# Performance work log

Hardware: AMD Instinct MI355X
Metric: run time of the kernel (lower is better)

The kernel has to match this reference:

```python
import jax, jax.numpy as jnp
import numpy as np

H = 32        # num_attention_heads
KVH = 8       # num_key_value_heads
D = 64        # head_dim
HID = 2048    # hidden_size
G = H // KVH  # num_key_value_groups


def setup_inputs() -> dict:
    key = jax.random.key(0)
    k1, k2, k3, k4, k5 = jax.random.split(key, 5)
    B, S = 1, 2048
    s = 1.0 / np.sqrt(HID)
    return {
        "hidden_states": jax.random.normal(k1, (B, S, HID), dtype=jnp.float32),
        "attention_mask": jnp.ones((B, S), dtype=jnp.int32),
        "Wq": jax.random.normal(k2, (H * D, HID), dtype=jnp.float32) * s,
        "Wk": jax.random.normal(k3, (KVH * D, HID), dtype=jnp.float32) * s,
        "Wv": jax.random.normal(k4, (KVH * D, HID), dtype=jnp.float32) * s,
        "Wo": jax.random.normal(k5, (HID, HID), dtype=jnp.float32) * s,
    }


def reference(hidden_states, attention_mask, Wq, Wk, Wv, Wo):
    B, S, _ = hidden_states.shape
    dtype = hidden_states.dtype

    q = (hidden_states @ Wq.T).reshape(B, S, H, D).transpose(0, 2, 1, 3)     # [B,H,S,D]
    k = (hidden_states @ Wk.T).reshape(B, S, KVH, D).transpose(0, 2, 1, 3)   # [B,KVH,S,D]
    v = (hidden_states @ Wv.T).reshape(B, S, KVH, D).transpose(0, 2, 1, 3)

    # repeat_interleave over head dim: each KV head serves G query heads
    k = jnp.repeat(k, G, axis=1)  # [B,H,S,D]
    v = jnp.repeat(v, G, axis=1)

    scores = jnp.einsum('bhqd,bhkd->bhqk', q, k) / np.sqrt(D)  # [B,H,S,S]

    causal = jnp.tril(jnp.ones((S, S), dtype=dtype))                # [S,S]
    am = attention_mask.astype(dtype)[:, None, None, :]              # [B,1,1,S]
    mask = am * causal[None, None, :, :]                             # [B,1,S,S]
    mask = (1.0 - mask) * jnp.finfo(dtype).min
    scores = scores + mask                                           # broadcast over heads

    weights = jax.nn.softmax(scores, axis=-1)
    attn = jnp.einsum('bhqk,bhkd->bhqd', weights, v)                 # [B,H,S,D]
    attn = attn.transpose(0, 2, 1, 3).reshape(B, S, HID)
    return attn @ Wo.T
```

## Files before the change

### kernel.cpp

```cpp
#include <hip/hip_runtime.h>
#include <hip/hip_bf16.h>
#include <math.h>

typedef __attribute__((ext_vector_type(4))) float f32x4;
typedef __attribute__((ext_vector_type(16))) float f32x16;
typedef __attribute__((ext_vector_type(8))) short bf16x8;
typedef __attribute__((ext_vector_type(4))) short s16x4;
typedef __attribute__((ext_vector_type(4))) unsigned int u32x4;
typedef __attribute__((ext_vector_type(2))) unsigned int u32x2;
typedef short s16;
typedef unsigned int u32;
typedef unsigned short u16;

#define S_LEN 2048
#define HIDN  2048
#define QKVW  3072
#define NH    32
#define NKVH  8
#define HD    64

__device__ __forceinline__ s16 f2bf(float f) {
  unsigned int u = __float_as_uint(f);
  unsigned int lsb = (u >> 16) & 1u;
  u += 0x7fffu + lsb;
  return (s16)(u >> 16);
}

__device__ __forceinline__ u32 cvtpk(float lo, float hi) {
  u32 r;
  asm("v_cvt_pk_bf16_f32 %0, %1, %2" : "=v"(r) : "v"(lo), "v"(hi));
  return r;
}

__device__ __forceinline__ void gload16(const void* g, void* l) {
  __builtin_amdgcn_global_load_lds(
      (const __attribute__((address_space(1))) void*)g,
      (__attribute__((address_space(3))) void*)l, 16, 0, 0);
}

__device__ __forceinline__ void pls(u32& a, u32& b) {
  asm volatile("v_permlane32_swap_b32 %0, %1" : "+v"(a), "+v"(b));
}

__device__ __forceinline__ int swz7(int row) { return (row ^ (row >> 3)) & 7; }

__global__ __launch_bounds__(256) void cvt_all(const float* __restrict__ h,
                                               const float* __restrict__ wq,
                                               const float* __restrict__ wk,
                                               const float* __restrict__ wv,
                                               const float* __restrict__ wo,
                                               s16x4* __restrict__ dst) {
  int i = blockIdx.x * 256 + threadIdx.x;
  const float* src; int off;
  if (i < 1048576)      { src = h;  off = i; }
  else if (i < 2097152) { src = wq; off = i - 1048576; }
  else if (i < 2359296) { src = wk; off = i - 2097152; }
  else if (i < 2621440) { src = wv; off = i - 2359296; }
  else                  { src = wo; off = i - 2621440; }
  if (i < 3670016) {
    float4 f = reinterpret_cast<const float4*>(src)[i < 1048576 ? i : off];
    s16x4 o;
    o.x = f2bf(f.x); o.y = f2bf(f.y); o.z = f2bf(f.z); o.w = f2bf(f.w);
    dst[i] = o;
  }
}

__device__ __forceinline__ void storeC(s16* C, size_t idx, float v)   { C[idx] = f2bf(v); }
__device__ __forceinline__ void storeC(float* C, size_t idx, float v) { C[idx] = v; }

template <typename OUT_T>
__global__ __launch_bounds__(512) void gemm_bt(const s16* __restrict__ A,
                                               const s16* __restrict__ B,
                                               OUT_T* __restrict__ C,
                                               int M, int N, int K) {
  __shared__ alignas(16) s16 As[2][8192];
  __shared__ alignas(16) s16 Bs[2][8192];

  const int t    = threadIdx.x;
  const int lane = t & 63;
  const int w    = t >> 6;
  const int wr   = (w >> 2) * 64;
  const int wc   = (w & 3) * 32;
  const int lr   = lane & 15;
  const int lg   = lane >> 4;
  const int bm   = blockIdx.y * 128;
  const int bn   = blockIdx.x * 128;

  const int srow0 = (w * 2) * 8 + (lane >> 3);
  const int srow1 = (w * 2 + 1) * 8 + (lane >> 3);
  const int sl0   = ((lane & 7) ^ swz7(srow0)) * 8;
  const int sl1   = ((lane & 7) ^ swz7(srow1)) * 8;

  f32x4 acc[4][2];
#pragma unroll
  for (int m = 0; m < 4; ++m)
#pragma unroll
    for (int n = 0; n < 2; ++n)
      acc[m][n] = (f32x4){0.f, 0.f, 0.f, 0.f};

  const int nK = K >> 6;
  int buf = 0;

  {
    gload16(&A[(size_t)(bm + srow0) * K + sl0], (char*)As[0] + (w * 2) * 1024);
    gload16(&A[(size_t)(bm + srow1) * K + sl1], (char*)As[0] + (w * 2 + 1) * 1024);
    gload16(&B[(size_t)(bn + srow0) * K + sl0], (char*)Bs[0] + (w * 2) * 1024);
    gload16(&B[(size_t)(bn + srow1) * K + sl1], (char*)Bs[0] + (w * 2 + 1) * 1024);
  }
  __syncthreads();

  for (int ki = 0; ki < nK; ++ki) {
    if (ki + 1 < nK) {
      const int kt = (ki + 1) << 6;
      gload16(&A[(size_t)(bm + srow0) * K + kt + sl0], (char*)As[buf ^ 1] + (w * 2) * 1024);
      gload16(&A[(size_t)(bm + srow1) * K + kt + sl1], (char*)As[buf ^ 1] + (w * 2 + 1) * 1024);
      gload16(&B[(size_t)(bn + srow0) * K + kt + sl0], (char*)Bs[buf ^ 1] + (w * 2) * 1024);
      gload16(&B[(size_t)(bn + srow1) * K + kt + sl1], (char*)Bs[buf ^ 1] + (w * 2 + 1) * 1024);
    }

    bf16x8 af[4][2], bfr[2][2];
#pragma unroll
    for (int kk = 0; kk < 2; ++kk) {
#pragma unroll
      for (int m = 0; m < 4; ++m) {
        int row = wr + m * 16 + lr;
        af[m][kk] = *(bf16x8*)((char*)As[buf] + row * 128 + (((kk * 4 + lg) ^ swz7(row)) << 4));
      }
#pragma unroll
      for (int n = 0; n < 2; ++n) {
        int row = wc + n * 16 + lr;
        bfr[n][kk] = *(bf16x8*)((char*)Bs[buf] + row * 128 + (((kk * 4 + lg) ^ swz7(row)) << 4));
      }
    }

    __builtin_amdgcn_s_setprio(1);
#pragma unroll
    for (int m = 0; m < 4; ++m)
#pragma unroll
      for (int n = 0; n < 2; ++n)
#pragma unroll
        for (int kk = 0; kk < 2; ++kk)
          acc[m][n] = __builtin_amdgcn_mfma_f32_16x16x32_bf16(af[m][kk], bfr[n][kk], acc[m][n], 0, 0, 0);
    __builtin_amdgcn_s_setprio(0);

    __syncthreads();
    buf ^= 1;
  }

#pragma unroll
  for (int m = 0; m < 4; ++m)
#pragma unroll
    for (int n = 0; n < 2; ++n) {
      int row = bm + wr + m * 16 + lg * 4;
      int col = bn + wc + n * 16 + lr;
#pragma unroll
      for (int j = 0; j < 4; ++j)
        storeC(C, (size_t)(row + j) * N + col, acc[m][n][j]);
    }
}

__global__ __launch_bounds__(256) void attn_kernel(
    const s16* __restrict__ QKV,
    const int* __restrict__ am,
    s16* __restrict__ Ob) {
  __shared__ alignas(16) char KsB[2][8192];
  __shared__ alignas(16) char VsB[2][8192];

  const int t    = threadIdx.x;
  const int lane = t & 63;
  const int w    = t >> 6;
  const int col  = lane & 31;
  const int hi   = lane >> 5;

  const int hk = blockIdx.x;
  const int qi = blockIdx.y;
  const int qt = (qi < 32) ? (63 - qi) : (qi - 32);
  const int h  = hk * 4 + w;
  const int nt = ((qt * 32 + 31) >> 6) + 1;
  const int kbase = 2048 + hk * 64;
  const int vbase = 2560 + hk * 64;

  const float CF = 0.18033688f;

  const int krow   = lane >> 3;
  const int kslotb = lane & 7;
  const int vkv    = 2 * (t >> 3);
  const int vd8    = (t & 7) * 8;

  const int qrow = qt * 32 + col;
  bf16x8 qf[4];
#pragma unroll
  for (int ds = 0; ds < 4; ++ds)
    qf[ds] = *(const bf16x8*)&QKV[(size_t)qrow * QKVW + h * 64 + ds * 16 + hi * 8];

  {
#pragma unroll
    for (int pp = 0; pp < 2; ++pp) {
      int c   = w * 2 + pp;
      int row = c * 8 + krow;
      int slot = kslotb ^ swz7(row);
      gload16(&QKV[(size_t)row * QKVW + kbase + slot * 8], KsB[0] + c * 1024);
    }
    bf16x8 va = *(const bf16x8*)&QKV[(size_t)vkv * QKVW + vbase + vd8];
    bf16x8 vb = *(const bf16x8*)&QKV[(size_t)(vkv + 1) * QKVW + vbase + vd8];
#pragma unroll
    for (int i = 0; i < 8; ++i) {
      int d = vd8 + i;
      u32 pk = (u32)(u16)va[i] | ((u32)(u16)vb[i] << 16);
      *(u32*)&VsB[0][(d * 128 + vkv * 2) ^ (swz7(d) << 4)] = pk;
    }
  }
  int acur = am[lane];

  float m_i = -1e30f, l_part = 0.f;
  f32x16 Oacc[2];
#pragma unroll
  for (int b = 0; b < 2; ++b)
#pragma unroll
    for (int i = 0; i < 16; ++i) Oacc[b][i] = 0.f;
  __syncthreads();

  for (int it = 0; it < nt; ++it) {
    const int cur = it & 1;
    const int kv0 = it * 64;
    const bool pre = (it + 1 < nt);

    bf16x8 va, vb;
    int anext = 0;
    if (pre) {
      const int nk0 = kv0 + 64;
#pragma unroll
      for (int pp = 0; pp < 2; ++pp) {
        int c   = w * 2 + pp;
        int row = c * 8 + krow;
        int slot = kslotb ^ swz7(row);
        gload16(&QKV[(size_t)(nk0 + row) * QKVW + kbase + slot * 8], KsB[cur ^ 1] + c * 1024);
      }
      va = *(const bf16x8*)&QKV[(size_t)(nk0 + vkv) * QKVW + vbase + vd8];
      vb = *(const bf16x8*)&QKV[(size_t)(nk0 + vkv + 1) * QKVW + vbase + vd8];
      anext = am[nk0 + lane];
    }

    f32x16 s0, s1;
#pragma unroll
    for (int i = 0; i < 16; ++i) { s0[i] = 0.f; s1[i] = 0.f; }
    __builtin_amdgcn_s_setprio(1);
#pragma unroll
    for (int ds = 0; ds < 4; ++ds) {
      int off = ds * 32 + hi * 16;
      bf16x8 k0 = *(bf16x8*)&KsB[cur][(col * 128 + off) ^ (swz7(col) << 4)];
      bf16x8 k1 = *(bf16x8*)&KsB[cur][((32 + col) * 128 + off) ^ (swz7(32 + col) << 4)];
      s0 = __builtin_amdgcn_mfma_f32_32x32x16_bf16(k0, qf[ds], s0, 0, 0, 0);
      s1 = __builtin_amdgcn_mfma_f32_32x32x16_bf16(k1, qf[ds], s1, 0, 0, 0);
    }
    __builtin_amdgcn_s_setprio(0);

    float pvv[32];
    unsigned long long m64 = __ballot(acur != 0);
    bool interior = (kv0 + 64 <= qt * 32) && (m64 == ~0ull);
    if (interior) {
#pragma unroll
      for (int r = 0; r < 16; ++r) { pvv[r] = s0[r] * CF; pvv[16 + r] = s1[r] * CF; }
    } else {
#pragma unroll
      for (int b = 0; b < 2; ++b)
#pragma unroll
        for (int r = 0; r < 16; ++r) {
          int kvl = b * 32 + (r & 3) + 8 * (r >> 2) + 4 * hi;
          float sv = b ? s1[r] : s0[r];
          bool ok = (kv0 + kvl <= qrow) && ((m64 >> kvl) & 1ull);
          pvv[b * 16 + r] = ok ? sv * CF : -INFINITY;
        }
    }

    float a0 = pvv[0], a1 = pvv[1], a2 = pvv[2], a3 = pvv[3];
#pragma unroll
    for (int i = 4; i < 32; i += 4) {
      a0 = fmaxf(a0, pvv[i]);     a1 = fmaxf(a1, pvv[i + 1]);
      a2 = fmaxf(a2, pvv[i + 2]); a3 = fmaxf(a3, pvv[i + 3]);
    }
    float lmax = fmaxf(fmaxf(a0, a1), fmaxf(a2, a3));
    lmax = fmaxf(lmax, __shfl_xor(lmax, 32));

    if (!__all(lmax - m_i <= 8.f)) {
      float nm = fmaxf(m_i, lmax);
      float al = __builtin_amdgcn_exp2f(m_i - nm);
      m_i = nm;
      l_part *= al;
#pragma unroll
      for (int b = 0; b < 2; ++b)
#pragma unroll
        for (int i = 0; i < 16; ++i) Oacc[b][i] *= al;
    }

    float t0 = 0.f, t1 = 0.f, t2 = 0.f, t3 = 0.f;
#pragma unroll
    for (int i = 0; i < 32; i += 4) {
      pvv[i]     = __builtin_amdgcn_exp2f(pvv[i] - m_i);     t0 += pvv[i];
      pvv[i + 1] = __builtin_amdgcn_exp2f(pvv[i + 1] - m_i); t1 += pvv[i + 1];
      pvv[i + 2] = __builtin_amdgcn_exp2f(pvv[i + 2] - m_i); t2 += pvv[i + 2];
      pvv[i + 3] = __builtin_amdgcn_exp2f(pvv[i + 3] - m_i); t3 += pvv[i + 3];
    }
    l_part += (t0 + t1) + (t2 + t3);

    bf16x8 pf[4];
#pragma unroll
    for (int b = 0; b < 2; ++b)
#pragma unroll
      for (int g = 0; g < 2; ++g) {
        int base = b * 16 + g * 8;
        u32 A1 = cvtpk(pvv[base + 0], pvv[base + 1]);
        u32 A2 = cvtpk(pvv[base + 2], pvv[base + 3]);
        u32 B1 = cvtpk(pvv[base + 4], pvv[base + 5]);
        u32 B2 = cvtpk(pvv[base + 6], pvv[base + 7]);
        pls(A1, B1);
        pls(A2, B2);
        u32x4 pw; pw[0] = A1; pw[1] = A2; pw[2] = B1; pw[3] = B2;
        pf[b * 2 + g] = *reinterpret_cast<bf16x8*>(&pw);
      }

    __builtin_amdgcn_s_setprio(1);
#pragma unroll
    for (int ks = 0; ks < 4; ++ks) {
      int off = ks * 32 + hi * 16;
#pragma unroll
      for (int db = 0; db < 2; ++db) {
        int d = db * 32 + col;
        bf16x8 vf = *(bf16x8*)&VsB[cur][(d * 128 + off) ^ (swz7(d) << 4)];
        Oacc[db] = __builtin_amdgcn_mfma_f32_32x32x16_bf16(vf, pf[ks], Oacc[db], 0, 0, 0);
      }
    }
    __builtin_amdgcn_s_setprio(0);

    if (pre) {
#pragma unroll
      for (int i = 0; i < 8; ++i) {
        int d = vd8 + i;
        u32 pk = (u32)(u16)va[i] | ((u32)(u16)vb[i] << 16);
        *(u32*)&VsB[cur ^ 1][(d * 128 + vkv * 2) ^ (swz7(d) << 4)] = pk;
      }
      acur = anext;
    }
    __syncthreads();
  }

  float l_i = l_part + __shfl_xor(l_part, 32);
  float linv = 1.0f / l_i;
#pragma unroll
  for (int db = 0; db < 2; ++db)
#pragma unroll
    for (int qd = 0; qd < 4; ++qd) {
      u32x2 o;
      o[0] = cvtpk(Oacc[db][qd * 4 + 0] * linv, Oacc[db][qd * 4 + 1] * linv);
      o[1] = cvtpk(Oacc[db][qd * 4 + 2] * linv, Oacc[db][qd * 4 + 3] * linv);
      int d0 = db * 32 + qd * 8 + hi * 4;
      *(u32x2*)&Ob[(size_t)qrow * HIDN + h * 64 + d0] = o;
    }
}

extern "C" void kernel_launch(void* const* d_in, const int* in_sizes, int n_in,
                              void* d_out, int out_size, void* d_ws, size_t ws_size,
                              hipStream_t stream) {
  const float* hidden = (const float*)d_in[0];
  const int*   am     = (const int*)d_in[1];
  const float* Wq     = (const float*)d_in[2];
  const float* Wk     = (const float*)d_in[3];
  const float* Wv     = (const float*)d_in[4];
  const float* Wo     = (const float*)d_in[5];
  float* out = (float*)d_out;

  s16* hb    = (s16*)d_ws;
  s16* wqkvb = hb    + 4194304;
  s16* wob   = wqkvb + 6291456;
  s16* QKVb  = wob   + 4194304;
  s16* Ab    = QKVb  + 6291456;

  cvt_all<<<14336, 256, 0, stream>>>(hidden, Wq, Wk, Wv, Wo, (s16x4*)d_ws);

  gemm_bt<s16><<<dim3(24, 16), 512, 0, stream>>>(hb, wqkvb, QKVb, 2048, 3072, 2048);

  attn_kernel<<<dim3(8, 64), 256, 0, stream>>>(QKVb, am, Ab);

  gemm_bt<float><<<dim3(16, 16), 512, 0, stream>>>(Ab, wob, out, 2048, 2048, 2048);
}
```

Measured before the change: 140.7 us.

## Split KV tiles across two wave groups per attention block and merge

The attention kernel now launches 512 threads per block. Two groups of four waves take alternating 64-row KV tiles, each with its own double-buffered K/V shared-memory region. At the end, group 0 writes its partial output, running max and sum to shared memory, and group 1 merges them with a log-sum-exp rescale before writing bf16 output. This halves the serial KV-loop length per block, which mainly helps the long causal rows, at the cost of double the LDS footprint, a final merge step and possibly lower block occupancy. A small cleanup also simplifies the source index in the fp32-to-bf16 conversion.

```diff
diff --git a/kernel.cpp b/kernel.cpp
--- a/kernel.cpp
+++ b/kernel.cpp
@@ -58,7 +58,7 @@
   else if (i < 2621440) { src = wv; off = i - 2359296; }
   else                  { src = wo; off = i - 2621440; }
   if (i < 3670016) {
-    float4 f = reinterpret_cast<const float4*>(src)[i < 1048576 ? i : off];
+    float4 f = reinterpret_cast<const float4*>(src)[off];
     s16x4 o;
     o.x = f2bf(f.x); o.y = f2bf(f.y); o.z = f2bf(f.z); o.w = f2bf(f.w);
     dst[i] = o;
@@ -159,16 +159,18 @@
     }
 }
 
-__global__ __launch_bounds__(256) void attn_kernel(
+__global__ __launch_bounds__(512) void attn_kernel(
     const s16* __restrict__ QKV,
     const int* __restrict__ am,
     s16* __restrict__ Ob) {
-  __shared__ alignas(16) char KsB[2][8192];
-  __shared__ alignas(16) char VsB[2][8192];
+  __shared__ alignas(16) char smem[65536];
+  __shared__ float2 mlb[4][64];
 
   const int t    = threadIdx.x;
+  const int g    = t >> 8;
+  const int tg   = t & 255;
   const int lane = t & 63;
-  const int w    = t >> 6;
+  const int w    = tg >> 6;
   const int col  = lane & 31;
   const int hi   = lane >> 5;
 
@@ -177,6 +179,7 @@
   const int qt = (qi < 32) ? (63 - qi) : (qi - 32);
   const int h  = hk * 4 + w;
   const int nt = ((qt * 32 + 31) >> 6) + 1;
+  const int R  = (nt + 1) >> 1;
   const int kbase = 2048 + hk * 64;
   const int vbase = 2560 + hk * 64;
 
@@ -184,8 +187,8 @@
 
   const int krow   = lane >> 3;
   const int kslotb = lane & 7;
-  const int vkv    = 2 * (t >> 3);
-  const int vd8    = (t & 7) * 8;
+  const int vkv    = 2 * (tg >> 3);
+  const int vd8    = (tg & 7) * 8;
 
   const int qrow = qt * 32 + col;
   bf16x8 qf[4];
@@ -193,24 +196,26 @@
   for (int ds = 0; ds < 4; ++ds)
     qf[ds] = *(const bf16x8*)&QKV[(size_t)qrow * QKVW + h * 64 + ds * 16 + hi * 8];
 
-  {
+  if (g < nt) {
+    char* Kn = smem + (g * 2 + 0) * 16384;
+    char* Vn = Kn + 8192;
 #pragma unroll
     for (int pp = 0; pp < 2; ++pp) {
       int c   = w * 2 + pp;
       int row = c * 8 + krow;
       int slot = kslotb ^ swz7(row);
-      gload16(&QKV[(size_t)row * QKVW + kbase + slot * 8], KsB[0] + c * 1024);
-    }
-    bf16x8 va = *(const bf16x8*)&QKV[(size_t)vkv * QKVW + vbase + vd8];
-    bf16x8 vb = *(const bf16x8*)&QKV[(size_t)(vkv + 1) * QKVW + vbase + vd8];
+      gload16(&QKV[(size_t)(g * 64 + row) * QKVW + kbase + slot * 8], Kn + c * 1024);
+    }
+    bf16x8 va = *(const bf16x8*)&QKV[(size_t)(g * 64 + vkv) * QKVW + vbase + vd8];
+    bf16x8 vb = *(const bf16x8*)&QKV[(size_t)(g * 64 + vkv + 1) * QKVW + vbase + vd8];
 #pragma unroll
     for (int i = 0; i < 8; ++i) {
       int d = vd8 + i;
       u32 pk = (u32)(u16)va[i] | ((u32)(u16)vb[i] << 16);
-      *(u32*)&VsB[0][(d * 128 + vkv * 2) ^ (swz7(d) << 4)] = pk;
-    }
-  }
-  int acur = am[lane];
+      *(u32*)&Vn[(d * 128 + vkv * 2) ^ (swz7(d) << 4)] = pk;
+    }
+  }
+  int acur = am[g * 64 + lane];
 
   float m_i = -1e30f, l_part = 0.f;
   f32x16 Oacc[2];
@@ -220,142 +225,173 @@
     for (int i = 0; i < 16; ++i) Oacc[b][i] = 0.f;
   __syncthreads();
 
-  for (int it = 0; it < nt; ++it) {
-    const int cur = it & 1;
-    const int kv0 = it * 64;
-    const bool pre = (it + 1 < nt);
+  for (int it = 0; it < R; ++it) {
+    const int buf  = it & 1;
+    const int tile = 2 * it + g;
+    const bool valid = (tile < nt);
+    const int kv0  = tile * 64;
+    const bool pre = (tile + 2 < nt);
+
+    char* Kc = smem + (g * 2 + buf) * 16384;
+    char* Vc = Kc + 8192;
+    char* Kn = smem + (g * 2 + (buf ^ 1)) * 16384;
+    char* Vn = Kn + 8192;
 
     bf16x8 va, vb;
     int anext = 0;
     if (pre) {
-      const int nk0 = kv0 + 64;
+      const int nk0 = kv0 + 128;
 #pragma unroll
       for (int pp = 0; pp < 2; ++pp) {
         int c   = w * 2 + pp;
         int row = c * 8 + krow;
         int slot = kslotb ^ swz7(row);
-        gload16(&QKV[(size_t)(nk0 + row) * QKVW + kbase + slot * 8], KsB[cur ^ 1] + c * 1024);
+        gload16(&QKV[(size_t)(nk0 + row) * QKVW + kbase + slot * 8], Kn + c * 1024);
       }
       va = *(const bf16x8*)&QKV[(size_t)(nk0 + vkv) * QKVW + vbase + vd8];
       vb = *(const bf16x8*)&QKV[(size_t)(nk0 + vkv + 1) * QKVW + vbase + vd8];
       anext = am[nk0 + lane];
     }
 
-    f32x16 s0, s1;
-#pragma unroll
-    for (int i = 0; i < 16; ++i) { s0[i] = 0.f; s1[i] = 0.f; }
-    __builtin_amdgcn_s_setprio(1);
-#pragma unroll
-    for (int ds = 0; ds < 4; ++ds) {
-      int off = ds * 32 + hi * 16;
-      bf16x8 k0 = *(bf16x8*)&KsB[cur][(col * 128 + off) ^ (swz7(col) << 4)];
-      bf16x8 k1 = *(bf16x8*)&KsB[cur][((32 + col) * 128 + off) ^ (swz7(32 + col) << 4)];
-      s0 = __builtin_amdgcn_mfma_f32_32x32x16_bf16(k0, qf[ds], s0, 0, 0, 0);
-      s1 = __builtin_amdgcn_mfma_f32_32x32x16_bf16(k1, qf[ds], s1, 0, 0, 0);
-    }
-    __builtin_amdgcn_s_setprio(0);
-
-    float pvv[32];
-    unsigned long long m64 = __ballot(acur != 0);
-    bool interior = (kv0 + 64 <= qt * 32) && (m64 == ~0ull);
-    if (interior) {
-#pragma unroll
-      for (int r = 0; r < 16; ++r) { pvv[r] = s0[r] * CF; pvv[16 + r] = s1[r] * CF; }
-    } else {
+    if (valid) {
+      f32x16 s0, s1;
+#pragma unroll
+      for (int i = 0; i < 16; ++i) { s0[i] = 0.f; s1[i] = 0.f; }
+      __builtin_amdgcn_s_setprio(1);
+#pragma unroll
+      for (int ds = 0; ds < 4; ++ds) {
+        int off = ds * 32 + hi * 16;
+        bf16x8 k0 = *(bf16x8*)&Kc[(col * 128 + off) ^ (swz7(col) << 4)];
+        bf16x8 k1 = *(bf16x8*)&Kc[((32 + col) * 128 + off) ^ (swz7(32 + col) << 4)];
+        s0 = __builtin_amdgcn_mfma_f32_32x32x16_bf16(k0, qf[ds], s0, 0, 0, 0);
+        s1 = __builtin_amdgcn_mfma_f32_32x32x16_bf16(k1, qf[ds], s1, 0, 0, 0);
+      }
+      __builtin_amdgcn_s_setprio(0);
+
+      float pvv[32];
+      unsigned long long m64 = __ballot(acur != 0);
+      bool interior = (kv0 + 64 <= qt * 32) && (m64 == ~0ull);
+      if (interior) {
+#pragma unroll
+        for (int r = 0; r < 16; ++r) { pvv[r] = s0[r] * CF; pvv[16 + r] = s1[r] * CF; }
+      } else {
+#pragma unroll
+        for (int b = 0; b < 2; ++b)
+#pragma unroll
+          for (int r = 0; r < 16; ++r) {
+            int kvl = b * 32 + (r & 3) + 8 * (r >> 2) + 4 * hi;
+            float sv = b ? s1[r] : s0[r];
+            bool ok = (kv0 + kvl <= qrow) && ((m64 >> kvl) & 1ull);
+            pvv[b * 16 + r] = ok ? sv * CF : -INFINITY;
+          }
+      }
+
+      float a0 = pvv[0], a1 = pvv[1], a2 = pvv[2], a3 = pvv[3];
+#pragma unroll
+      for (int i = 4; i < 32; i += 4) {
+        a0 = fmaxf(a0, pvv[i]);     a1 = fmaxf(a1, pvv[i + 1]);
+        a2 = fmaxf(a2, pvv[i + 2]); a3 = fmaxf(a3, pvv[i + 3]);
+      }
+      float lmax = fmaxf(fmaxf(a0, a1), fmaxf(a2, a3));
+      lmax = fmaxf(lmax, __shfl_xor(lmax, 32));
+
+      if (!__all(lmax - m_i <= 8.f)) {
+        float nm = fmaxf(m_i, lmax);
+        float al = __builtin_amdgcn_exp2f(m_i - nm);
+        m_i = nm;
+        l_part *= al;
+#pragma unroll
+        for (int b = 0; b < 2; ++b)
+#pragma unroll
+          for (int i = 0; i < 16; ++i) Oacc[b][i] *= al;
+      }
+
+      float t0 = 0.f, t1 = 0.f, t2 = 0.f, t3 = 0.f;
+#pragma unroll
+      for (int i = 0; i < 32; i += 4) {
+        pvv[i]     = __builtin_amdgcn_exp2f(pvv[i] - m_i);     t0 += pvv[i];
+        pvv[i + 1] = __builtin_amdgcn_exp2f(pvv[i + 1] - m_i); t1 += pvv[i + 1];
+        pvv[i + 2] = __builtin_amdgcn_exp2f(pvv[i + 2] - m_i); t2 += pvv[i + 2];
+        pvv[i + 3] = __builtin_amdgcn_exp2f(pvv[i + 3] - m_i); t3 += pvv[i + 3];
+      }
+      l_part += (t0 + t1) + (t2 + t3);
+
+      bf16x8 pf[4];
 #pragma unroll
       for (int b = 0; b < 2; ++b)
 #pragma unroll
-        for (int r = 0; r < 16; ++r) {
-          int kvl = b * 32 + (r & 3) + 8 * (r >> 2) + 4 * hi;
-          float sv = b ? s1[r] : s0[r];
-          bool ok = (kv0 + kvl <= qrow) && ((m64 >> kvl) & 1ull);
-          pvv[b * 16 + r] = ok ? sv * CF : -INFINITY;
+        for (int gg = 0; gg < 2; ++gg) {
+          int base = b * 16 + gg * 8;
+          u32 A1 = cvtpk(pvv[base + 0], pvv[base + 1]);
+          u32 A2 = cvtpk(pvv[base + 2], pvv[base + 3]);
+          u32 B1 = cvtpk(pvv[base + 4], pvv[base + 5]);
+          u32 B2 = cvtpk(pvv[base + 6], pvv[base + 7]);
+          pls(A1, B1);
+          pls(A2, B2);
+          u32x4 pw; pw[0] = A1; pw[1] = A2; pw[2] = B1; pw[3] = B2;
+          pf[b * 2 + gg] = *reinterpret_cast<bf16x8*>(&pw);
         }
-    }
-
-    float a0 = pvv[0], a1 = pvv[1], a2 = pvv[2], a3 = pvv[3];
-#pragma unroll
-    for (int i = 4; i < 32; i += 4) {
-      a0 = fmaxf(a0, pvv[i]);     a1 = fmaxf(a1, pvv[i + 1]);
-      a2 = fmaxf(a2, pvv[i + 2]); a3 = fmaxf(a3, pvv[i + 3]);
-    }
-    float lmax = fmaxf(fmaxf(a0, a1), fmaxf(a2, a3));
-    lmax = fmaxf(lmax, __shfl_xor(lmax, 32));
-
-    if (!__all(lmax - m_i <= 8.f)) {
-      float nm = fmaxf(m_i, lmax);
-      float al = __builtin_amdgcn_exp2f(m_i - nm);
-      m_i = nm;
-      l_part *= al;
-#pragma unroll
-      for (int b = 0; b < 2; ++b)
-#pragma unroll
-        for (int i = 0; i < 16; ++i) Oacc[b][i] *= al;
-    }
-
-    float t0 = 0.f, t1 = 0.f, t2 = 0.f, t3 = 0.f;
-#pragma unroll
-    for (int i = 0; i < 32; i += 4) {
-      pvv[i]     = __builtin_amdgcn_exp2f(pvv[i] - m_i);     t0 += pvv[i];
-      pvv[i + 1] = __builtin_amdgcn_exp2f(pvv[i + 1] - m_i); t1 += pvv[i + 1];
-      pvv[i + 2] = __builtin_amdgcn_exp2f(pvv[i + 2] - m_i); t2 += pvv[i + 2];
-      pvv[i + 3] = __builtin_amdgcn_exp2f(pvv[i + 3] - m_i); t3 += pvv[i + 3];
-    }
-    l_part += (t0 + t1) + (t2 + t3);
-
-    bf16x8 pf[4];
-#pragma unroll
-    for (int b = 0; b < 2; ++b)
-#pragma unroll
-      for (int g = 0; g < 2; ++g) {
-        int base = b * 16 + g * 8;
-        u32 A1 = cvtpk(pvv[base + 0], pvv[base + 1]);
-        u32 A2 = cvtpk(pvv[base + 2], pvv[base + 3]);
-        u32 B1 = cvtpk(pvv[base + 4], pvv[base + 5]);
-        u32 B2 = cvtpk(pvv[base + 6], pvv[base + 7]);
-        pls(A1, B1);
-        pls(A2, B2);
-        u32x4 pw; pw[0] = A1; pw[1] = A2; pw[2] = B1; pw[3] = B2;
-        pf[b * 2 + g] = *reinterpret_cast<bf16x8*>(&pw);
-      }
-
-    __builtin_amdgcn_s_setprio(1);
-#pragma unroll
-    for (int ks = 0; ks < 4; ++ks) {
-      int off = ks * 32 + hi * 16;
-#pragma unroll
-      for (int db = 0; db < 2; ++db) {
-        int d = db * 32 + col;
-        bf16x8 vf = *(bf16x8*)&VsB[cur][(d * 128 + off) ^ (swz7(d) << 4)];
-        Oacc[db] = __builtin_amdgcn_mfma_f32_32x32x16_bf16(vf, pf[ks], Oacc[db], 0, 0, 0);
-      }
-    }
-    __builtin_amdgcn_s_setprio(0);
+
+      __builtin_amdgcn_s_setprio(1);
+#pragma unroll
+      for (int ks = 0; ks < 4; ++ks) {
+        int off = ks * 32 + hi * 16;
+#pragma unroll
+        for (int db = 0; db < 2; ++db) {
+          int d = db * 32 + col;
+          bf16x8 vf = *(bf16x8*)&Vc[(d * 128 + off) ^ (swz7(d) << 4)];
+          Oacc[db] = __builtin_amdgcn_mfma_f32_32x32x16_bf16(vf, pf[ks], Oacc[db], 0, 0, 0);
+        }
+      }
+      __builtin_amdgcn_s_setprio(0);
+    }
 
     if (pre) {
 #pragma unroll
       for (int i = 0; i < 8; ++i) {
         int d = vd8 + i;
         u32 pk = (u32)(u16)va[i] | ((u32)(u16)vb[i] << 16);
-        *(u32*)&VsB[cur ^ 1][(d * 128 + vkv * 2) ^ (swz7(d) << 4)] = pk;
+        *(u32*)&Vn[(d * 128 + vkv * 2) ^ (swz7(d) << 4)] = pk;
       }
       acur = anext;
     }
     __syncthreads();
   }
 
-  float l_i = l_part + __shfl_xor(l_part, 32);
-  float linv = 1.0f / l_i;
-#pragma unroll
-  for (int db = 0; db < 2; ++db)
-#pragma unroll
-    for (int qd = 0; qd < 4; ++qd) {
-      u32x2 o;
-      o[0] = cvtpk(Oacc[db][qd * 4 + 0] * linv, Oacc[db][qd * 4 + 1] * linv);
-      o[1] = cvtpk(Oacc[db][qd * 4 + 2] * linv, Oacc[db][qd * 4 + 3] * linv);
-      int d0 = db * 32 + qd * 8 + hi * 4;
-      *(u32x2*)&Ob[(size_t)qrow * HIDN + h * 64 + d0] = o;
-    }
+  float l_p = l_part + __shfl_xor(l_part, 32);
+
+  if (g == 0) {
+    float* pool = (float*)smem + w * 2048 + lane * 32;
+#pragma unroll
+    for (int b = 0; b < 2; ++b)
+#pragma unroll
+      for (int i = 0; i < 16; ++i) pool[b * 16 + i] = Oacc[b][i];
+    mlb[w][lane] = make_float2(m_i, l_p);
+  }
+  __syncthreads();
+  if (g == 1) {
+    const float* pool = (const float*)smem + w * 2048 + lane * 32;
+    float2 ml0 = mlb[w][lane];
+    float mm = fmaxf(ml0.x, m_i);
+    float b0 = __builtin_amdgcn_exp2f(ml0.x - mm);
+    float b1 = __builtin_amdgcn_exp2f(m_i - mm);
+    float linv = 1.0f / (ml0.y * b0 + l_p * b1);
+    float s0 = b0 * linv, s1v = b1 * linv;
+#pragma unroll
+    for (int db = 0; db < 2; ++db)
+#pragma unroll
+      for (int qd = 0; qd < 4; ++qd) {
+        float o0 = pool[db * 16 + qd * 4 + 0] * s0 + Oacc[db][qd * 4 + 0] * s1v;
+        float o1 = pool[db * 16 + qd * 4 + 1] * s0 + Oacc[db][qd * 4 + 1] * s1v;
+        float o2 = pool[db * 16 + qd * 4 + 2] * s0 + Oacc[db][qd * 4 + 2] * s1v;
+        float o3 = pool[db * 16 + qd * 4 + 3] * s0 + Oacc[db][qd * 4 + 3] * s1v;
+        u32x2 o;
+        o[0] = cvtpk(o0, o1);
+        o[1] = cvtpk(o2, o3);
+        int d0 = db * 32 + qd * 8 + hi * 4;
+        *(u32x2*)&Ob[(size_t)qrow * HIDN + h * 64 + d0] = o;
+      }
+  }
 }
 
 extern "C" void kernel_launch(void* const* d_in, const int* in_sizes, int n_in,
@@ -379,7 +415,7 @@
 
   gemm_bt<s16><<<dim3(24, 16), 512, 0, stream>>>(hb, wqkvb, QKVb, 2048, 3072, 2048);
 
-  attn_kernel<<<dim3(8, 64), 256, 0, stream>>>(QKVb, am, Ab);
+  attn_kernel<<<dim3(8, 64), 512, 0, stream>>>(QKVb, am, Ab);
 
   gemm_bt<float><<<dim3(16, 16), 512, 0, stream>>>(Ab, wob, out, 2048, 2048, 2048);
 }
```

Measured after the change: 140.7 us. Within noise of the previous version (+0.0%).

## Split long causal attention rows across two KV chunks with a merge kernel

Applied to the files above, without the earlier changes.

Attention for query tiles needing more than 16 KV tiles is split into two KV-range blocks (split-K / flash-decoding style). Each block writes an unnormalized bf16 partial output plus its running max and sum, and a new merge kernel combines the two. This balances per-block work under causal masking and adds parallelism, at the cost of an extra launch and partial-result traffic. The score scaling is also folded into an FMA inside the exp, and launch bounds now request more waves per SIMD.

```diff
diff --git a/kernel.cpp b/kernel.cpp
--- a/kernel.cpp
+++ b/kernel.cpp
@@ -24,6 +24,10 @@
   unsigned int lsb = (u >> 16) & 1u;
   u += 0x7fffu + lsb;
   return (s16)(u >> 16);
+}
+
+__device__ __forceinline__ float bf2f(s16 x) {
+  return __uint_as_float(((u32)(u16)x) << 16);
 }
 
 __device__ __forceinline__ u32 cvtpk(float lo, float hi) {
@@ -58,7 +62,7 @@
   else if (i < 2621440) { src = wv; off = i - 2359296; }
   else                  { src = wo; off = i - 2621440; }
   if (i < 3670016) {
-    float4 f = reinterpret_cast<const float4*>(src)[i < 1048576 ? i : off];
+    float4 f = reinterpret_cast<const float4*>(src)[off];
     s16x4 o;
     o.x = f2bf(f.x); o.y = f2bf(f.y); o.z = f2bf(f.z); o.w = f2bf(f.w);
     dst[i] = o;
@@ -159,10 +163,12 @@
     }
 }
 
-__global__ __launch_bounds__(256) void attn_kernel(
+__global__ __launch_bounds__(256, 4) void attn_part(
     const s16* __restrict__ QKV,
     const int* __restrict__ am,
-    s16* __restrict__ Ob) {
+    s16* __restrict__ Ob,
+    s16* __restrict__ partO,
+    float2* __restrict__ partML) {
   __shared__ alignas(16) char KsB[2][8192];
   __shared__ alignas(16) char VsB[2][8192];
 
@@ -172,14 +178,18 @@
   const int col  = lane & 31;
   const int hi   = lane >> 5;
 
-  const int hk = blockIdx.x;
-  const int qi = blockIdx.y;
-  const int qt = (qi < 32) ? (63 - qi) : (qi - 32);
+  const int hk  = blockIdx.x;
+  const int qt  = 63 - (int)blockIdx.y;
+  const int ck  = blockIdx.z;
+  const int nt  = (qt >> 1) + 1;
+  const int nck = (nt + 15) >> 4;
+  if (ck >= nck) return;
+  const int tt0 = ck * 16;
+  const int tt1 = (nt < tt0 + 16) ? nt : (tt0 + 16);
+
   const int h  = hk * 4 + w;
-  const int nt = ((qt * 32 + 31) >> 6) + 1;
   const int kbase = 2048 + hk * 64;
   const int vbase = 2560 + hk * 64;
-
   const float CF = 0.18033688f;
 
   const int krow   = lane >> 3;
@@ -194,15 +204,16 @@
     qf[ds] = *(const bf16x8*)&QKV[(size_t)qrow * QKVW + h * 64 + ds * 16 + hi * 8];
 
   {
+    const int k0 = tt0 * 64;
 #pragma unroll
     for (int pp = 0; pp < 2; ++pp) {
       int c   = w * 2 + pp;
       int row = c * 8 + krow;
       int slot = kslotb ^ swz7(row);
-      gload16(&QKV[(size_t)row * QKVW + kbase + slot * 8], KsB[0] + c * 1024);
-    }
-    bf16x8 va = *(const bf16x8*)&QKV[(size_t)vkv * QKVW + vbase + vd8];
-    bf16x8 vb = *(const bf16x8*)&QKV[(size_t)(vkv + 1) * QKVW + vbase + vd8];
+      gload16(&QKV[(size_t)(k0 + row) * QKVW + kbase + slot * 8], KsB[0] + c * 1024);
+    }
+    bf16x8 va = *(const bf16x8*)&QKV[(size_t)(k0 + vkv) * QKVW + vbase + vd8];
+    bf16x8 vb = *(const bf16x8*)&QKV[(size_t)(k0 + vkv + 1) * QKVW + vbase + vd8];
 #pragma unroll
     for (int i = 0; i < 8; ++i) {
       int d = vd8 + i;
@@ -210,7 +221,7 @@
       *(u32*)&VsB[0][(d * 128 + vkv * 2) ^ (swz7(d) << 4)] = pk;
     }
   }
-  int acur = am[lane];
+  int acur = am[tt0 * 64 + lane];
 
   float m_i = -1e30f, l_part = 0.f;
   f32x16 Oacc[2];
@@ -220,10 +231,10 @@
     for (int i = 0; i < 16; ++i) Oacc[b][i] = 0.f;
   __syncthreads();
 
-  for (int it = 0; it < nt; ++it) {
-    const int cur = it & 1;
+  for (int it = tt0; it < tt1; ++it) {
+    const int cur = (it - tt0) & 1;
     const int kv0 = it * 64;
-    const bool pre = (it + 1 < nt);
+    const bool pre = (it + 1 < tt1);
 
     bf16x8 va, vb;
     int anext = 0;
@@ -260,7 +271,7 @@
     bool interior = (kv0 + 64 <= qt * 32) && (m64 == ~0ull);
     if (interior) {
 #pragma unroll
-      for (int r = 0; r < 16; ++r) { pvv[r] = s0[r] * CF; pvv[16 + r] = s1[r] * CF; }
+      for (int r = 0; r < 16; ++r) { pvv[r] = s0[r]; pvv[16 + r] = s1[r]; }
     } else {
 #pragma unroll
       for (int b = 0; b < 2; ++b)
@@ -269,7 +280,7 @@
           int kvl = b * 32 + (r & 3) + 8 * (r >> 2) + 4 * hi;
           float sv = b ? s1[r] : s0[r];
           bool ok = (kv0 + kvl <= qrow) && ((m64 >> kvl) & 1ull);
-          pvv[b * 16 + r] = ok ? sv * CF : -INFINITY;
+          pvv[b * 16 + r] = ok ? sv : -INFINITY;
         }
     }
 
@@ -281,9 +292,10 @@
     }
     float lmax = fmaxf(fmaxf(a0, a1), fmaxf(a2, a3));
     lmax = fmaxf(lmax, __shfl_xor(lmax, 32));
-
-    if (!__all(lmax - m_i <= 8.f)) {
-      float nm = fmaxf(m_i, lmax);
+    float lmaxs = lmax * CF;
+
+    if (!__all(lmaxs - m_i <= 8.f)) {
+      float nm = fmaxf(m_i, lmaxs);
       float al = __builtin_amdgcn_exp2f(m_i - nm);
       m_i = nm;
       l_part *= al;
@@ -296,10 +308,10 @@
     float t0 = 0.f, t1 = 0.f, t2 = 0.f, t3 = 0.f;
 #pragma unroll
     for (int i = 0; i < 32; i += 4) {
-      pvv[i]     = __builtin_amdgcn_exp2f(pvv[i] - m_i);     t0 += pvv[i];
-      pvv[i + 1] = __builtin_amdgcn_exp2f(pvv[i + 1] - m_i); t1 += pvv[i + 1];
-      pvv[i + 2] = __builtin_amdgcn_exp2f(pvv[i + 2] - m_i); t2 += pvv[i + 2];
-      pvv[i + 3] = __builtin_amdgcn_exp2f(pvv[i + 3] - m_i); t3 += pvv[i + 3];
+      pvv[i]     = __builtin_amdgcn_exp2f(__builtin_fmaf(pvv[i],     CF, -m_i)); t0 += pvv[i];
+      pvv[i + 1] = __builtin_amdgcn_exp2f(__builtin_fmaf(pvv[i + 1], CF, -m_i)); t1 += pvv[i + 1];
+      pvv[i + 2] = __builtin_amdgcn_exp2f(__builtin_fmaf(pvv[i + 2], CF, -m_i)); t2 += pvv[i + 2];
+      pvv[i + 3] = __builtin_amdgcn_exp2f(__builtin_fmaf(pvv[i + 3], CF, -m_i)); t3 += pvv[i + 3];
     }
     l_part += (t0 + t1) + (t2 + t3);
 
@@ -307,8 +319,8 @@
 #pragma unroll
     for (int b = 0; b < 2; ++b)
 #pragma unroll
-      for (int g = 0; g < 2; ++g) {
-        int base = b * 16 + g * 8;
+      for (int gg = 0; gg < 2; ++gg) {
+        int base = b * 16 + gg * 8;
         u32 A1 = cvtpk(pvv[base + 0], pvv[base + 1]);
         u32 A2 = cvtpk(pvv[base + 2], pvv[base + 3]);
         u32 B1 = cvtpk(pvv[base + 4], pvv[base + 5]);
@@ -316,7 +328,7 @@
         pls(A1, B1);
         pls(A2, B2);
         u32x4 pw; pw[0] = A1; pw[1] = A2; pw[2] = B1; pw[3] = B2;
-        pf[b * 2 + g] = *reinterpret_cast<bf16x8*>(&pw);
+        pf[b * 2 + gg] = *reinterpret_cast<bf16x8*>(&pw);
       }
 
     __builtin_amdgcn_s_setprio(1);
@@ -345,17 +357,61 @@
   }
 
   float l_i = l_part + __shfl_xor(l_part, 32);
-  float linv = 1.0f / l_i;
-#pragma unroll
-  for (int db = 0; db < 2; ++db)
-#pragma unroll
-    for (int qd = 0; qd < 4; ++qd) {
-      u32x2 o;
-      o[0] = cvtpk(Oacc[db][qd * 4 + 0] * linv, Oacc[db][qd * 4 + 1] * linv);
-      o[1] = cvtpk(Oacc[db][qd * 4 + 2] * linv, Oacc[db][qd * 4 + 3] * linv);
-      int d0 = db * 32 + qd * 8 + hi * 4;
-      *(u32x2*)&Ob[(size_t)qrow * HIDN + h * 64 + d0] = o;
-    }
+  if (nck == 1) {
+    float linv = 1.0f / l_i;
+#pragma unroll
+    for (int db = 0; db < 2; ++db)
+#pragma unroll
+      for (int qd = 0; qd < 4; ++qd) {
+        u32x2 o;
+        o[0] = cvtpk(Oacc[db][qd * 4 + 0] * linv, Oacc[db][qd * 4 + 1] * linv);
+        o[1] = cvtpk(Oacc[db][qd * 4 + 2] * linv, Oacc[db][qd * 4 + 3] * linv);
+        int d0 = db * 32 + qd * 8 + hi * 4;
+        *(u32x2*)&Ob[(size_t)qrow * HIDN + h * 64 + d0] = o;
+      }
+  } else {
+    size_t slot = ((size_t)((qt - 32) * 32 + col) * 32 + h) * 2 + ck;
+    s16* po = partO + slot * 64;
+#pragma unroll
+    for (int db = 0; db < 2; ++db)
+#pragma unroll
+      for (int qd = 0; qd < 4; ++qd) {
+        u32x2 o;
+        o[0] = cvtpk(Oacc[db][qd * 4 + 0], Oacc[db][qd * 4 + 1]);
+        o[1] = cvtpk(Oacc[db][qd * 4 + 2], Oacc[db][qd * 4 + 3]);
+        int d0 = db * 32 + qd * 8 + hi * 4;
+        *(u32x2*)&po[d0] = o;
+      }
+    if (hi == 0) partML[slot] = make_float2(m_i, l_i);
+  }
+}
+
+__global__ __launch_bounds__(256) void attn_merge(
+    const s16* __restrict__ partO, const float2* __restrict__ partML,
+    s16* __restrict__ Ob) {
+  int gid = blockIdx.x * 256 + threadIdx.x;
+  int r = gid >> 5;
+  int h = gid & 31;
+  size_t s0 = ((size_t)r * 32 + h) * 2;
+  float2 ml0 = partML[s0], ml1 = partML[s0 + 1];
+  float mm = fmaxf(ml0.x, ml1.x);
+  float b0 = __builtin_amdgcn_exp2f(ml0.x - mm);
+  float b1 = __builtin_amdgcn_exp2f(ml1.x - mm);
+  float linv = 1.0f / (ml0.y * b0 + ml1.y * b1);
+  b0 *= linv; b1 *= linv;
+  const s16* p0 = partO + s0 * 64;
+  const s16* p1 = partO + (s0 + 1) * 64;
+  s16* dst = Ob + (size_t)(1024 + r) * HIDN + h * 64;
+#pragma unroll
+  for (int d8 = 0; d8 < 64; d8 += 8) {
+    bf16x8 a = *(const bf16x8*)&p0[d8];
+    bf16x8 b = *(const bf16x8*)&p1[d8];
+    bf16x8 o;
+#pragma unroll
+    for (int i = 0; i < 8; ++i)
+      o[i] = f2bf(bf2f(a[i]) * b0 + bf2f(b[i]) * b1);
+    *(bf16x8*)&dst[d8] = o;
+  }
 }
 
 extern "C" void kernel_launch(void* const* d_in, const int* in_sizes, int n_in,
@@ -374,12 +430,15 @@
   s16* wob   = wqkvb + 6291456;
   s16* QKVb  = wob   + 4194304;
   s16* Ab    = QKVb  + 6291456;
+  s16* partO = Ab    + 4194304;
+  float2* partML = (float2*)(partO + 4194304);
 
   cvt_all<<<14336, 256, 0, stream>>>(hidden, Wq, Wk, Wv, Wo, (s16x4*)d_ws);
 
   gemm_bt<s16><<<dim3(24, 16), 512, 0, stream>>>(hb, wqkvb, QKVb, 2048, 3072, 2048);
 
-  attn_kernel<<<dim3(8, 64), 256, 0, stream>>>(QKVb, am, Ab);
+  attn_part<<<dim3(8, 64, 2), 256, 0, stream>>>(QKVb, am, Ab, partO, partML);
+  attn_merge<<<128, 256, 0, stream>>>(partO, partML, Ab);
 
   gemm_bt<float><<<dim3(16, 16), 512, 0, stream>>>(Ab, wob, out, 2048, 2048, 2048);
 }
```

Result: slower. 194.9 us (+38.5%).
